# Optimization experiments

Measured on AMD Instinct MI355X. Metric: run time of the kernel, lower is better.

The kernel has to match this reference:

```python
import jax, jax.numpy as jnp
import numpy as np

B, S, H, DIN, DOUT = 4, 2048, 8, 128, 128


def setup_inputs() -> dict:
    key = jax.random.key(0)
    ks = jax.random.split(key, 11)
    sc = 0.05
    return {
        "q": jax.random.normal(ks[0], (B, S, DIN), jnp.float32),
        "k": jax.random.normal(ks[1], (B, S, DIN), jnp.float32),
        "v": jax.random.normal(ks[2], (B, S, DOUT), jnp.float32),
        "Wq": jax.random.normal(ks[3], (DIN, DIN * H), jnp.float32) * sc,
        "bq": jax.random.normal(ks[4], (DIN * H,), jnp.float32) * sc,
        "Wk": jax.random.normal(ks[5], (DIN, DIN * H), jnp.float32) * sc,
        "bk": jax.random.normal(ks[6], (DIN * H,), jnp.float32) * sc,
        "Wv": jax.random.normal(ks[7], (DOUT, DOUT * H), jnp.float32) * sc,
        "bv": jax.random.normal(ks[8], (DOUT * H,), jnp.float32) * sc,
        "Wo": jax.random.normal(ks[9], (H * DOUT, DOUT), jnp.float32) * sc,
        "bo": jax.random.normal(ks[10], (DOUT,), jnp.float32) * sc,
    }


def reference(q, k, v, Wq, bq, Wk, bk, Wv, bv, Wo, bo):
    b, s, din = q.shape
    dout = v.shape[-1]
    h = Wq.shape[1] // din
    # project and split heads: [B, S, H, D] -> [B, H, S, D]
    qs = (q @ Wq + bq).reshape(b, s, h, din).transpose(0, 2, 1, 3)
    kh = (k @ Wk + bk).reshape(b, k.shape[1], h, din).transpose(0, 2, 1, 3)
    vh = (v @ Wv + bv).reshape(b, v.shape[1], h, dout).transpose(0, 2, 1, 3)
    # scaled dot-product attention; note the original scales by sqrt(input_dim)
    scale = 1.0 / jnp.sqrt(jnp.asarray(din, q.dtype))
    scores = jnp.einsum("bhqd,bhkd->bhqk", qs, kh) * scale
    attn = jax.nn.softmax(scores, axis=-1)
    out = jnp.einsum("bhqk,bhkd->bhqd", attn, vh)  # [B, H, S, Dout]
    out = out.transpose(0, 2, 1, 3).reshape(b, s, h * dout)
    return out @ Wo + bo
```

## Files before the change

kernel.cpp:

```cpp
#include <hip/hip_runtime.h>
#include <hip/hip_bf16.h>
#include <stdint.h>

typedef __bf16 bf16_t;
typedef bf16_t bf16x8 __attribute__((ext_vector_type(8)));
typedef bf16_t bf16x4 __attribute__((ext_vector_type(4)));
typedef float  f32x4  __attribute__((ext_vector_type(4)));

#define MFMA_BF16 __builtin_amdgcn_mfma_f32_16x16x32_bf16

constexpr int BB = 4, SS = 2048, HH = 8;
constexpr float QK_SCALE = 0.08838834764831845f;
constexpr float LOG2E    = 1.4426950408889634f;
constexpr float QSCL     = QK_SCALE * LOG2E;

__device__ __forceinline__ float exp2_fast(float x) {
#if __has_builtin(__builtin_amdgcn_exp2f)
    return __builtin_amdgcn_exp2f(x);
#else
    return __expf(x * 0.6931471805599453f);
#endif
}

__device__ __forceinline__ void dma16(const bf16_t* g, bf16_t* l) {
    __builtin_amdgcn_global_load_lds(
        (const __attribute__((address_space(1))) void*)g,
        (__attribute__((address_space(3))) void*)l, 16, 0, 0);
}

__global__ void prep_kernel(const float* __restrict__ q, const float* __restrict__ k,
                            const float* __restrict__ v,
                            const float* __restrict__ Wq, const float* __restrict__ Wk,
                            const float* __restrict__ Wv, const float* __restrict__ Wo,
                            bf16_t* __restrict__ WqT, bf16_t* __restrict__ WkT,
                            bf16_t* __restrict__ WvT, bf16_t* __restrict__ WoT,
                            bf16_t* __restrict__ Abf)
{
    int bid = blockIdx.x, t = threadIdx.x;
    if (bid < 128) {
        __shared__ float tile[64][65];
        int m = bid >> 5, tl = bid & 31;
        const float* src; bf16_t* dst; int R, C, tr, tc; float scale = 1.0f;
        if (m < 3) {
            src = (m == 0) ? Wq : (m == 1) ? Wk : Wv;
            dst = (m == 0) ? WqT : (m == 1) ? WkT : WvT;
            R = 128; C = 1024; tr = tl >> 4; tc = tl & 15;
            if (m == 0) scale = QSCL;
        } else {
            src = Wo; dst = WoT; R = 1024; C = 128; tr = tl >> 1; tc = tl & 1;
        }
        int r0 = tr * 64, c0 = tc * 64;
        int rr = t >> 2, cc = (t & 3) * 16;
        const float4* s4 = (const float4*)(src + (size_t)(r0 + rr) * C + c0 + cc);
        #pragma unroll
        for (int i = 0; i < 4; ++i) {
            float4 f = s4[i];
            tile[rr][cc + 4 * i + 0] = f.x; tile[rr][cc + 4 * i + 1] = f.y;
            tile[rr][cc + 4 * i + 2] = f.z; tile[rr][cc + 4 * i + 3] = f.w;
        }
        __syncthreads();
        bf16x8 o0, o1;
        #pragma unroll
        for (int i = 0; i < 8; ++i) o0[i] = (bf16_t)(tile[cc + i][rr] * scale);
        #pragma unroll
        for (int i = 0; i < 8; ++i) o1[i] = (bf16_t)(tile[cc + 8 + i][rr] * scale);
        bf16_t* d = dst + (size_t)(c0 + rr) * R + r0 + cc;
        *(bf16x8*)d = o0;
        *(bf16x8*)(d + 8) = o1;
    } else {
        int bid2 = bid - 128;
        size_t base = (size_t)bid2 * 4096 + t * 16;
        int z = (int)(base >> 20);
        size_t off = base & 1048575;
        const float* s = (z == 0) ? q : (z == 1) ? k : v;
        const float4* s4 = (const float4*)(s + off);
        bf16_t* d = Abf + (size_t)z * 1048576 + off;
        float4 f0 = s4[0], f1 = s4[1], f2 = s4[2], f3 = s4[3];
        bf16x8 p0 = { (bf16_t)f0.x, (bf16_t)f0.y, (bf16_t)f0.z, (bf16_t)f0.w,
                      (bf16_t)f1.x, (bf16_t)f1.y, (bf16_t)f1.z, (bf16_t)f1.w };
        bf16x8 p1 = { (bf16_t)f2.x, (bf16_t)f2.y, (bf16_t)f2.z, (bf16_t)f2.w,
                      (bf16_t)f3.x, (bf16_t)f3.y, (bf16_t)f3.z, (bf16_t)f3.w };
        *(bf16x8*)d = p0;
        *(bf16x8*)(d + 8) = p1;
    }
}

__global__ __launch_bounds__(256, 2)
void proj_kernel(const bf16_t* __restrict__ Abf,
                 const bf16_t* __restrict__ WqT, const bf16_t* __restrict__ WkT,
                 const bf16_t* __restrict__ WvT,
                 const float* __restrict__ bq, const float* __restrict__ bk,
                 const float* __restrict__ bv,
                 bf16_t* __restrict__ Qh, bf16_t* __restrict__ Kh, bf16_t* __restrict__ VhT)
{
    __shared__ __align__(16) bf16_t a_s[2][128 * 64];
    __shared__ __align__(16) bf16_t b_s[2][128 * 64];
    const int z = blockIdx.z;
    const bf16_t* A    = Abf + (size_t)z * 1048576;
    const bf16_t* BT   = (z == 0) ? WqT : (z == 1) ? WkT : WvT;
    const float*  bias = (z == 0) ? bq  : (z == 1) ? bk  : bv;
    const float   bscale = (z == 0) ? QSCL : 1.0f;
    const int t = threadIdx.x, w = t >> 6, lane = t & 63, q = lane >> 4, ln = lane & 15;
    const int m0 = blockIdx.x * 128;
    const int n0 = blockIdx.y * 128;
    const int wm = (w & 1) * 64, wn = (w >> 1) * 64;

    auto stage = [&](int buf, int kb) {
        #pragma unroll
        for (int j = 0; j < 4; ++j) {
            int row = w * 32 + j * 8 + (lane >> 3);
            int u = (lane & 7) ^ (row & 7);
            dma16(A + (size_t)(m0 + row) * 128 + kb * 64 + u * 8,
                  &a_s[buf][(w * 32 + j * 8) * 64]);
            dma16(BT + (size_t)(n0 + row) * 128 + kb * 64 + u * 8,
                  &b_s[buf][(w * 32 + j * 8) * 64]);
        }
    };

    f32x4 acc[4][4] = {};
    stage(0, 0);
    __syncthreads();
    stage(1, 1);
    #pragma unroll
    for (int kb = 0; kb < 2; ++kb) {
        if (kb == 1) __syncthreads();
        const bf16_t* as = a_s[kb];
        const bf16_t* bs = b_s[kb];
        #pragma unroll
        for (int kc = 0; kc < 2; ++kc) {
            bf16x8 af[4], bfr[4];
            #pragma unroll
            for (int mi = 0; mi < 4; ++mi)
                af[mi] = *(const bf16x8*)&as[(wm + mi * 16 + ln) * 64 + (((kc * 4 + q) ^ (ln & 7)) * 8)];
            #pragma unroll
            for (int ni = 0; ni < 4; ++ni)
                bfr[ni] = *(const bf16x8*)&bs[(wn + ni * 16 + ln) * 64 + (((kc * 4 + q) ^ (ln & 7)) * 8)];
            if (z != 2) {
                #pragma unroll
                for (int mi = 0; mi < 4; ++mi)
                    #pragma unroll
                    for (int ni = 0; ni < 4; ++ni)
                        acc[mi][ni] = MFMA_BF16(af[mi], bfr[ni], acc[mi][ni], 0, 0, 0);
            } else {
                #pragma unroll
                for (int mi = 0; mi < 4; ++mi)
                    #pragma unroll
                    for (int ni = 0; ni < 4; ++ni)
                        acc[mi][ni] = MFMA_BF16(bfr[ni], af[mi], acc[mi][ni], 0, 0, 0);
            }
        }
    }
    bf16_t* out = (z == 0) ? Qh : (z == 1) ? Kh : VhT;
    if (z != 2) {
        #pragma unroll
        for (int ni = 0; ni < 4; ++ni) {
            int col = n0 + wn + ni * 16 + ln;
            int h = col >> 7, d = col & 127;
            float bvv = bias[col] * bscale;
            #pragma unroll
            for (int mi = 0; mi < 4; ++mi) {
                int mbase = m0 + wm + mi * 16 + q * 4;
                int b = mbase >> 11, s = mbase & 2047;
                #pragma unroll
                for (int r = 0; r < 4; ++r)
                    out[((size_t)(b * HH + h) * SS + (s + r)) * 128 + d] =
                        (bf16_t)(acc[mi][ni][r] + bvv);
            }
        }
    } else {
        #pragma unroll
        for (int ni = 0; ni < 4; ++ni) {
            #pragma unroll
            for (int r = 0; r < 4; ++r) {
                int col = n0 + wn + ni * 16 + q * 4 + r;
                int h = col >> 7, d = col & 127;
                float bvv = bias[col];
                #pragma unroll
                for (int mi = 0; mi < 4; ++mi) {
                    int mg = m0 + wm + mi * 16 + ln;
                    int b = mg >> 11, s = mg & 2047;
                    out[((size_t)(b * HH + h) * 128 + d) * SS + s] =
                        (bf16_t)(acc[mi][ni][r] + bvv);
                }
            }
        }
    }
}

__global__ __launch_bounds__(256, 2)
void attn_kernel(const bf16_t* __restrict__ Qh, const bf16_t* __restrict__ Kh,
                 const bf16_t* __restrict__ VhT, bf16_t* __restrict__ Aout)
{
    __shared__ __align__(16) bf16_t k_s[2][64 * 128];
    __shared__ __align__(16) bf16_t v_s[2][128 * 64];
    __shared__ __align__(16) bf16_t p_s[4 * 32 * 64];
    const int t = threadIdx.x;
    const int w = t >> 6, lane = t & 63, q = lane >> 4, ln = lane & 15;
    const int bh = blockIdx.y;
    const int q0 = blockIdx.x * 128;
    const size_t hb = (size_t)bh * SS * 128;

    bf16x8 qf[2][4];
    #pragma unroll
    for (int rg = 0; rg < 2; ++rg) {
        const bf16_t* qrow = Qh + hb + (size_t)(q0 + w * 32 + rg * 16 + ln) * 128;
        #pragma unroll
        for (int kc = 0; kc < 4; ++kc)
            qf[rg][kc] = *(const bf16x8*)(qrow + kc * 32 + q * 8);
    }
    const bf16_t one = (bf16_t)1.0f;
    bf16x8 ones = { one, one, one, one, one, one, one, one };
    f32x4 o[2][8] = {};
    f32x4 ol[2] = {};
    bf16_t* pw = &p_s[w * 32 * 64];

    auto stage = [&](int buf, int kv0) {
        #pragma unroll
        for (int j = 0; j < 4; ++j) {
            int row = w * 16 + j * 4 + (lane >> 4);
            int blk = (lane & 15) ^ (row & 7);
            dma16(Kh + hb + (size_t)(kv0 + row) * 128 + blk * 8,
                  &k_s[buf][(w * 16 + j * 4) * 128]);
        }
        #pragma unroll
        for (int j = 0; j < 4; ++j) {
            int row = w * 32 + j * 8 + (lane >> 3);
            int blk = (lane & 7) ^ (row & 7);
            dma16(VhT + hb + (size_t)row * SS + kv0 + blk * 8,
                  &v_s[buf][(w * 32 + j * 8) * 64]);
        }
    };

    stage(0, 0);
    for (int it = 0; it < SS / 64; ++it) {
        int cur = it & 1;
        __syncthreads();
        if (it + 1 < SS / 64) stage(cur ^ 1, (it + 1) * 64);
        const bf16_t* ks = &k_s[cur][0];
        const bf16_t* vs = &v_s[cur][0];
        f32x4 sc[2][4] = {};
        #pragma unroll
        for (int kc = 0; kc < 4; ++kc) {
            #pragma unroll
            for (int nt = 0; nt < 4; ++nt) {
                int row = nt * 16 + ln;
                bf16x8 kf = *(const bf16x8*)&ks[row * 128 + (((kc * 4 + q) ^ (ln & 7)) * 8)];
                sc[0][nt] = MFMA_BF16(kf, qf[0][kc], sc[0][nt], 0, 0, 0);
                sc[1][nt] = MFMA_BF16(kf, qf[1][kc], sc[1][nt], 0, 0, 0);
            }
        }
        #pragma unroll
        for (int rg = 0; rg < 2; ++rg) {
            #pragma unroll
            for (int nt = 0; nt < 4; ++nt) {
                bf16x4 pk;
                #pragma unroll
                for (int r = 0; r < 4; ++r)
                    pk[r] = (bf16_t)exp2_fast(sc[rg][nt][r]);
                int row = rg * 16 + ln;
                int blk = (2 * nt + (q >> 1)) ^ (row & 7);
                *(bf16x4*)&pw[row * 64 + blk * 8 + (q & 1) * 4] = pk;
            }
        }
        #pragma unroll
        for (int c2 = 0; c2 < 2; ++c2) {
            int pblk = (c2 * 4 + q) ^ (ln & 7);
            bf16x8 pf0 = *(const bf16x8*)&pw[ln * 64 + pblk * 8];
            bf16x8 pf1 = *(const bf16x8*)&pw[(16 + ln) * 64 + pblk * 8];
            ol[0] = MFMA_BF16(pf0, ones, ol[0], 0, 0, 0);
            ol[1] = MFMA_BF16(pf1, ones, ol[1], 0, 0, 0);
            #pragma unroll
            for (int dt = 0; dt < 8; ++dt) {
                int vrow = dt * 16 + ln;
                bf16x8 vf = *(const bf16x8*)&vs[vrow * 64 + (((c2 * 4 + q) ^ (ln & 7)) * 8)];
                o[0][dt] = MFMA_BF16(pf0, vf, o[0][dt], 0, 0, 0);
                o[1][dt] = MFMA_BF16(pf1, vf, o[1][dt], 0, 0, 0);
            }
        }
    }
    const int b = bh >> 3, h = bh & 7;
    #pragma unroll
    for (int rg = 0; rg < 2; ++rg) {
        #pragma unroll
        for (int r = 0; r < 4; ++r) {
            float inv = 1.0f / ol[rg][r];
            int s = q0 + w * 32 + rg * 16 + q * 4 + r;
            bf16_t* dst = Aout + ((size_t)(b * SS + s)) * 1024 + h * 128;
            #pragma unroll
            for (int dt = 0; dt < 8; ++dt)
                dst[dt * 16 + ln] = (bf16_t)(o[rg][dt][r] * inv);
        }
    }
}

__global__ __launch_bounds__(256, 2)
void out_gemm(const bf16_t* __restrict__ A, const bf16_t* __restrict__ BT,
              const float* __restrict__ bias, float* __restrict__ out)
{
    __shared__ __align__(16) bf16_t a_s[2][32 * 64];
    __shared__ __align__(16) bf16_t b_s[2][128 * 64];
    const int t = threadIdx.x, w = t >> 6, lane = t & 63, q = lane >> 4, ln = lane & 15;
    const int m0 = blockIdx.x * 32;
    const int mh = (w & 1) * 16, nh = (w >> 1) * 64;
    f32x4 acc[4] = {};

    auto stage = [&](int buf, int kk) {
        {
            int row = w * 8 + (lane >> 3);
            int u = (lane & 7) ^ (row & 7);
            dma16(A + (size_t)(m0 + row) * 1024 + kk + u * 8, &a_s[buf][(w * 8) * 64]);
        }
        #pragma unroll
        for (int j = 0; j < 4; ++j) {
            int row = w * 32 + j * 8 + (lane >> 3);
            int u = (lane & 7) ^ (row & 7);
            dma16(BT + (size_t)row * 1024 + kk + u * 8, &b_s[buf][(w * 32 + j * 8) * 64]);
        }
    };

    stage(0, 0);
    for (int kb = 0; kb < 16; ++kb) {
        __syncthreads();
        if (kb < 15) stage((kb + 1) & 1, (kb + 1) * 64);
        const bf16_t* as = a_s[kb & 1];
        const bf16_t* bs = b_s[kb & 1];
        #pragma unroll
        for (int kc = 0; kc < 2; ++kc) {
            bf16x8 af = *(const bf16x8*)&as[(mh + ln) * 64 + (((kc * 4 + q) ^ (ln & 7)) * 8)];
            #pragma unroll
            for (int ni = 0; ni < 4; ++ni) {
                int brow = nh + ni * 16 + ln;
                bf16x8 bfr = *(const bf16x8*)&bs[brow * 64 + (((kc * 4 + q) ^ (ln & 7)) * 8)];
                acc[ni] = MFMA_BF16(af, bfr, acc[ni], 0, 0, 0);
            }
        }
    }
    #pragma unroll
    for (int ni = 0; ni < 4; ++ni) {
        int col = nh + ni * 16 + ln;
        float bv = bias[col];
        #pragma unroll
        for (int r = 0; r < 4; ++r)
            out[(size_t)(m0 + mh + q * 4 + r) * 128 + col] = acc[ni][r] + bv;
    }
}

extern "C" void kernel_launch(void* const* d_in, const int* in_sizes, int n_in,
                              void* d_out, int out_size, void* d_ws, size_t ws_size,
                              hipStream_t stream)
{
    const float* q  = (const float*)d_in[0];
    const float* k  = (const float*)d_in[1];
    const float* v  = (const float*)d_in[2];
    const float* Wq = (const float*)d_in[3];
    const float* bq = (const float*)d_in[4];
    const float* Wk = (const float*)d_in[5];
    const float* bk = (const float*)d_in[6];
    const float* Wv = (const float*)d_in[7];
    const float* bv = (const float*)d_in[8];
    const float* Wo = (const float*)d_in[9];
    const float* bo = (const float*)d_in[10];
    float* out = (float*)d_out;

    char* ws = (char*)d_ws;
    bf16_t* WqT  = (bf16_t*)(ws + 0 * (1 << 18));
    bf16_t* WkT  = (bf16_t*)(ws + 1 * (1 << 18));
    bf16_t* WvT  = (bf16_t*)(ws + 2 * (1 << 18));
    bf16_t* WoT  = (bf16_t*)(ws + 3 * (1 << 18));
    bf16_t* Abf  = (bf16_t*)(ws + (1 << 20));
    bf16_t* Qh   = (bf16_t*)(ws + (1 << 23));
    bf16_t* Kh   = (bf16_t*)(ws + (1 << 23) + 1 * (1 << 24));
    bf16_t* VhT  = (bf16_t*)(ws + (1 << 23) + 2 * (1 << 24));
    bf16_t* Aout = (bf16_t*)(ws + (1 << 23) + 3 * (1 << 24));

    prep_kernel<<<896, 256, 0, stream>>>(q, k, v, Wq, Wk, Wv, Wo,
                                         WqT, WkT, WvT, WoT, Abf);
    proj_kernel<<<dim3(64, 8, 3), 256, 0, stream>>>(Abf, WqT, WkT, WvT,
                                                    bq, bk, bv, Qh, Kh, VhT);
    attn_kernel<<<dim3(SS / 128, BB * HH), 256, 0, stream>>>(Qh, Kh, VhT, Aout);
    out_gemm<<<256, 256, 0, stream>>>(Aout, WoT, bo, out);
}
```

Before: 185.6 us.

## Use 32x32 MFMA in attention with 256-query tiles and LDS-staged projection stores

The attention kernel moves from 16x16x32 to 32x32x16 bf16 MFMA, with each wave handling 64 query rows and each block 256. The row sum is accumulated in registers from the exponentials, replacing the extra ones-MFMA. The projection kernel now stages its output tile through LDS so global stores are coalesced 16-byte vectors, including the transposed V layout. The aim is to raise MFMA efficiency and cut scattered store traffic, at the cost of a larger register footprint, occupancy lowered to one block, and fewer blocks in the grid.

```diff
diff --git a/kernel.cpp b/kernel.cpp
--- a/kernel.cpp
+++ b/kernel.cpp
@@ -6,8 +6,10 @@
 typedef bf16_t bf16x8 __attribute__((ext_vector_type(8)));
 typedef bf16_t bf16x4 __attribute__((ext_vector_type(4)));
 typedef float  f32x4  __attribute__((ext_vector_type(4)));
+typedef float  f32x16 __attribute__((ext_vector_type(16)));
 
 #define MFMA_BF16 __builtin_amdgcn_mfma_f32_16x16x32_bf16
+#define MFMA32    __builtin_amdgcn_mfma_f32_32x32x16_bf16
 
 constexpr int BB = 4, SS = 2048, HH = 8;
 constexpr float QK_SCALE = 0.08838834764831845f;
@@ -93,8 +95,7 @@
                  const float* __restrict__ bv,
                  bf16_t* __restrict__ Qh, bf16_t* __restrict__ Kh, bf16_t* __restrict__ VhT)
 {
-    __shared__ __align__(16) bf16_t a_s[2][128 * 64];
-    __shared__ __align__(16) bf16_t b_s[2][128 * 64];
+    __shared__ __align__(16) bf16_t smem[2 * 2 * 128 * 64];
     const int z = blockIdx.z;
     const bf16_t* A    = Abf + (size_t)z * 1048576;
     const bf16_t* BT   = (z == 0) ? WqT : (z == 1) ? WkT : WvT;
@@ -106,14 +107,16 @@
     const int wm = (w & 1) * 64, wn = (w >> 1) * 64;
 
     auto stage = [&](int buf, int kb) {
+        bf16_t* as = smem + buf * 16384;
+        bf16_t* bs = smem + buf * 16384 + 8192;
         #pragma unroll
         for (int j = 0; j < 4; ++j) {
             int row = w * 32 + j * 8 + (lane >> 3);
             int u = (lane & 7) ^ (row & 7);
             dma16(A + (size_t)(m0 + row) * 128 + kb * 64 + u * 8,
-                  &a_s[buf][(w * 32 + j * 8) * 64]);
+                  &as[(w * 32 + j * 8) * 64]);
             dma16(BT + (size_t)(n0 + row) * 128 + kb * 64 + u * 8,
-                  &b_s[buf][(w * 32 + j * 8) * 64]);
+                  &bs[(w * 32 + j * 8) * 64]);
         }
     };
 
@@ -124,8 +127,8 @@
     #pragma unroll
     for (int kb = 0; kb < 2; ++kb) {
         if (kb == 1) __syncthreads();
-        const bf16_t* as = a_s[kb];
-        const bf16_t* bs = b_s[kb];
+        const bf16_t* as = smem + kb * 16384;
+        const bf16_t* bs = smem + kb * 16384 + 8192;
         #pragma unroll
         for (int kc = 0; kc < 2; ++kc) {
             bf16x8 af[4], bfr[4];
@@ -135,160 +138,170 @@
             #pragma unroll
             for (int ni = 0; ni < 4; ++ni)
                 bfr[ni] = *(const bf16x8*)&bs[(wn + ni * 16 + ln) * 64 + (((kc * 4 + q) ^ (ln & 7)) * 8)];
-            if (z != 2) {
+            #pragma unroll
+            for (int mi = 0; mi < 4; ++mi)
                 #pragma unroll
-                for (int mi = 0; mi < 4; ++mi)
-                    #pragma unroll
-                    for (int ni = 0; ni < 4; ++ni)
-                        acc[mi][ni] = MFMA_BF16(af[mi], bfr[ni], acc[mi][ni], 0, 0, 0);
-            } else {
-                #pragma unroll
-                for (int mi = 0; mi < 4; ++mi)
-                    #pragma unroll
-                    for (int ni = 0; ni < 4; ++ni)
-                        acc[mi][ni] = MFMA_BF16(bfr[ni], af[mi], acc[mi][ni], 0, 0, 0);
-            }
-        }
-    }
-    bf16_t* out = (z == 0) ? Qh : (z == 1) ? Kh : VhT;
-    if (z != 2) {
-        #pragma unroll
-        for (int ni = 0; ni < 4; ++ni) {
-            int col = n0 + wn + ni * 16 + ln;
-            int h = col >> 7, d = col & 127;
-            float bvv = bias[col] * bscale;
-            #pragma unroll
-            for (int mi = 0; mi < 4; ++mi) {
-                int mbase = m0 + wm + mi * 16 + q * 4;
-                int b = mbase >> 11, s = mbase & 2047;
-                #pragma unroll
-                for (int r = 0; r < 4; ++r)
-                    out[((size_t)(b * HH + h) * SS + (s + r)) * 128 + d] =
-                        (bf16_t)(acc[mi][ni][r] + bvv);
-            }
-        }
-    } else {
-        #pragma unroll
-        for (int ni = 0; ni < 4; ++ni) {
+                for (int ni = 0; ni < 4; ++ni)
+                    acc[mi][ni] = MFMA_BF16(af[mi], bfr[ni], acc[mi][ni], 0, 0, 0);
+        }
+    }
+    __syncthreads();
+    bf16_t* tb = smem;
+    #pragma unroll
+    for (int ni = 0; ni < 4; ++ni) {
+        int col = wn + ni * 16 + ln;
+        float bvv = bias[n0 + col] * bscale;
+        #pragma unroll
+        for (int mi = 0; mi < 4; ++mi) {
             #pragma unroll
             for (int r = 0; r < 4; ++r) {
-                int col = n0 + wn + ni * 16 + q * 4 + r;
-                int h = col >> 7, d = col & 127;
-                float bvv = bias[col];
-                #pragma unroll
-                for (int mi = 0; mi < 4; ++mi) {
-                    int mg = m0 + wm + mi * 16 + ln;
-                    int b = mg >> 11, s = mg & 2047;
-                    out[((size_t)(b * HH + h) * 128 + d) * SS + s] =
-                        (bf16_t)(acc[mi][ni][r] + bvv);
-                }
-            }
-        }
-    }
-}
-
-__global__ __launch_bounds__(256, 2)
+                int rowm = wm + mi * 16 + q * 4 + r;
+                bf16_t val = (bf16_t)(acc[mi][ni][r] + bvv);
+                if (z != 2) tb[rowm * 136 + col] = val;
+                else        tb[col * 136 + rowm] = val;
+            }
+        }
+    }
+    __syncthreads();
+    {
+        int row = t >> 1, half = t & 1;
+        const bf16_t* src = tb + row * 136 + half * 64;
+        const int b = m0 >> 11, s0 = m0 & 2047, h = n0 >> 7;
+        bf16_t* dst;
+        if (z != 2)
+            dst = ((z == 0) ? Qh : Kh) + ((size_t)((b * HH + h) * SS) + s0 + row) * 128 + half * 64;
+        else
+            dst = VhT + ((size_t)((b * HH + h) * 128 + row)) * SS + s0 + half * 64;
+        #pragma unroll
+        for (int i = 0; i < 8; ++i)
+            *(bf16x8*)(dst + i * 8) = *(const bf16x8*)(src + i * 8);
+    }
+}
+
+__global__ __launch_bounds__(256, 1)
 void attn_kernel(const bf16_t* __restrict__ Qh, const bf16_t* __restrict__ Kh,
                  const bf16_t* __restrict__ VhT, bf16_t* __restrict__ Aout)
 {
     __shared__ __align__(16) bf16_t k_s[2][64 * 128];
     __shared__ __align__(16) bf16_t v_s[2][128 * 64];
-    __shared__ __align__(16) bf16_t p_s[4 * 32 * 64];
+    __shared__ __align__(16) bf16_t p_s[4][64 * 64];
+    __shared__ float l_lds[4][64];
     const int t = threadIdx.x;
-    const int w = t >> 6, lane = t & 63, q = lane >> 4, ln = lane & 15;
+    const int w = t >> 6, lane = t & 63;
+    const int hh = lane >> 5, l31 = lane & 31;
     const int bh = blockIdx.y;
-    const int q0 = blockIdx.x * 128;
+    const int q0 = blockIdx.x * 256;
+    const int qw0 = q0 + w * 64;
     const size_t hb = (size_t)bh * SS * 128;
 
-    bf16x8 qf[2][4];
-    #pragma unroll
-    for (int rg = 0; rg < 2; ++rg) {
-        const bf16_t* qrow = Qh + hb + (size_t)(q0 + w * 32 + rg * 16 + ln) * 128;
-        #pragma unroll
-        for (int kc = 0; kc < 4; ++kc)
-            qf[rg][kc] = *(const bf16x8*)(qrow + kc * 32 + q * 8);
-    }
-    const bf16_t one = (bf16_t)1.0f;
-    bf16x8 ones = { one, one, one, one, one, one, one, one };
-    f32x4 o[2][8] = {};
-    f32x4 ol[2] = {};
-    bf16_t* pw = &p_s[w * 32 * 64];
+    bf16x8 qf[2][8];
+    #pragma unroll
+    for (int ni = 0; ni < 2; ++ni) {
+        const bf16_t* qrow = Qh + hb + (size_t)(qw0 + ni * 32 + l31) * 128 + hh * 8;
+        #pragma unroll
+        for (int c = 0; c < 8; ++c)
+            qf[ni][c] = *(const bf16x8*)(qrow + c * 16);
+    }
+    f32x16 o[2][4] = {};
+    float lsum[2] = {0.f, 0.f};
+    bf16_t* pw = p_s[w];
 
     auto stage = [&](int buf, int kv0) {
         #pragma unroll
         for (int j = 0; j < 4; ++j) {
             int row = w * 16 + j * 4 + (lane >> 4);
-            int blk = (lane & 15) ^ (row & 7);
-            dma16(Kh + hb + (size_t)(kv0 + row) * 128 + blk * 8,
+            int u = (lane & 15) ^ (row & 15);
+            dma16(Kh + hb + (size_t)(kv0 + row) * 128 + u * 8,
                   &k_s[buf][(w * 16 + j * 4) * 128]);
         }
         #pragma unroll
         for (int j = 0; j < 4; ++j) {
             int row = w * 32 + j * 8 + (lane >> 3);
-            int blk = (lane & 7) ^ (row & 7);
-            dma16(VhT + hb + (size_t)row * SS + kv0 + blk * 8,
+            int u = (lane & 7) ^ (row & 7);
+            dma16(VhT + hb + (size_t)row * SS + kv0 + u * 8,
                   &v_s[buf][(w * 32 + j * 8) * 64]);
         }
     };
 
     stage(0, 0);
     for (int it = 0; it < SS / 64; ++it) {
-        int cur = it & 1;
+        const int cur = it & 1;
         __syncthreads();
         if (it + 1 < SS / 64) stage(cur ^ 1, (it + 1) * 64);
-        const bf16_t* ks = &k_s[cur][0];
-        const bf16_t* vs = &v_s[cur][0];
-        f32x4 sc[2][4] = {};
-        #pragma unroll
-        for (int kc = 0; kc < 4; ++kc) {
-            #pragma unroll
-            for (int nt = 0; nt < 4; ++nt) {
-                int row = nt * 16 + ln;
-                bf16x8 kf = *(const bf16x8*)&ks[row * 128 + (((kc * 4 + q) ^ (ln & 7)) * 8)];
-                sc[0][nt] = MFMA_BF16(kf, qf[0][kc], sc[0][nt], 0, 0, 0);
-                sc[1][nt] = MFMA_BF16(kf, qf[1][kc], sc[1][nt], 0, 0, 0);
-            }
-        }
-        #pragma unroll
-        for (int rg = 0; rg < 2; ++rg) {
-            #pragma unroll
-            for (int nt = 0; nt < 4; ++nt) {
-                bf16x4 pk;
+        const bf16_t* ks = k_s[cur];
+        const bf16_t* vs = v_s[cur];
+
+        #pragma unroll
+        for (int mi = 0; mi < 2; ++mi) {
+            const int krow = mi * 32 + l31;
+            const bf16_t* kb = ks + krow * 128;
+            const int ksw = krow & 15;
+            f32x16 s0 = {}, s1 = {};
+            #pragma unroll
+            for (int c = 0; c < 8; ++c) {
+                bf16x8 kf = *(const bf16x8*)&kb[((2 * c + hh) ^ ksw) * 8];
+                s0 = MFMA32(kf, qf[0][c], s0, 0, 0, 0);
+                s1 = MFMA32(kf, qf[1][c], s1, 0, 0, 0);
+            }
+            const int psw = l31 & 7;
+            #pragma unroll
+            for (int ni = 0; ni < 2; ++ni) {
+                const f32x16 sv = ni ? s1 : s0;
+                bf16_t* prow = pw + (ni * 32 + l31) * 64 + hh * 4;
+                float ls = 0.f;
                 #pragma unroll
-                for (int r = 0; r < 4; ++r)
-                    pk[r] = (bf16_t)exp2_fast(sc[rg][nt][r]);
-                int row = rg * 16 + ln;
-                int blk = (2 * nt + (q >> 1)) ^ (row & 7);
-                *(bf16x4*)&pw[row * 64 + blk * 8 + (q & 1) * 4] = pk;
-            }
-        }
-        #pragma unroll
-        for (int c2 = 0; c2 < 2; ++c2) {
-            int pblk = (c2 * 4 + q) ^ (ln & 7);
-            bf16x8 pf0 = *(const bf16x8*)&pw[ln * 64 + pblk * 8];
-            bf16x8 pf1 = *(const bf16x8*)&pw[(16 + ln) * 64 + pblk * 8];
-            ol[0] = MFMA_BF16(pf0, ones, ol[0], 0, 0, 0);
-            ol[1] = MFMA_BF16(pf1, ones, ol[1], 0, 0, 0);
-            #pragma unroll
-            for (int dt = 0; dt < 8; ++dt) {
-                int vrow = dt * 16 + ln;
-                bf16x8 vf = *(const bf16x8*)&vs[vrow * 64 + (((c2 * 4 + q) ^ (ln & 7)) * 8)];
-                o[0][dt] = MFMA_BF16(pf0, vf, o[0][dt], 0, 0, 0);
-                o[1][dt] = MFMA_BF16(pf1, vf, o[1][dt], 0, 0, 0);
-            }
-        }
-    }
-    const int b = bh >> 3, h = bh & 7;
-    #pragma unroll
-    for (int rg = 0; rg < 2; ++rg) {
-        #pragma unroll
-        for (int r = 0; r < 4; ++r) {
-            float inv = 1.0f / ol[rg][r];
-            int s = q0 + w * 32 + rg * 16 + q * 4 + r;
-            bf16_t* dst = Aout + ((size_t)(b * SS + s)) * 1024 + h * 128;
-            #pragma unroll
-            for (int dt = 0; dt < 8; ++dt)
-                dst[dt * 16 + ln] = (bf16_t)(o[rg][dt][r] * inv);
+                for (int g = 0; g < 4; ++g) {
+                    bf16x4 pk;
+                    #pragma unroll
+                    for (int r = 0; r < 4; ++r) {
+                        float e = exp2_fast(sv[g * 4 + r]);
+                        ls += e;
+                        pk[r] = (bf16_t)e;
+                    }
+                    *(bf16x4*)&prow[((mi * 4 + g) ^ psw) * 8] = pk;
+                }
+                lsum[ni] += ls;
+            }
+        }
+        #pragma unroll
+        for (int c = 0; c < 4; ++c) {
+            bf16x8 vf[4];
+            #pragma unroll
+            for (int ni = 0; ni < 4; ++ni) {
+                int drow = ni * 32 + l31;
+                vf[ni] = *(const bf16x8*)&vs[drow * 64 + (((2 * c + hh) ^ (drow & 7)) * 8)];
+            }
+            #pragma unroll
+            for (int mp = 0; mp < 2; ++mp) {
+                int prow = mp * 32 + l31;
+                bf16x8 pf = *(const bf16x8*)&pw[prow * 64 + (((2 * c + hh) ^ (prow & 7)) * 8)];
+                #pragma unroll
+                for (int ni = 0; ni < 4; ++ni)
+                    o[mp][ni] = MFMA32(pf, vf[ni], o[mp][ni], 0, 0, 0);
+            }
+        }
+    }
+    lsum[0] += __shfl_xor(lsum[0], 32);
+    lsum[1] += __shfl_xor(lsum[1], 32);
+    if (hh == 0) {
+        l_lds[w][l31] = lsum[0];
+        l_lds[w][32 + l31] = lsum[1];
+    }
+    const int b = bh >> 3, hd = bh & 7;
+    #pragma unroll
+    for (int mp = 0; mp < 2; ++mp) {
+        #pragma unroll
+        for (int g = 0; g < 4; ++g) {
+            #pragma unroll
+            for (int r = 0; r < 4; ++r) {
+                int qrl = mp * 32 + g * 8 + hh * 4 + r;
+                float inv = 1.0f / l_lds[w][qrl];
+                int s = qw0 + qrl;
+                bf16_t* dst = Aout + ((size_t)(b * SS + s)) * 1024 + hd * 128;
+                #pragma unroll
+                for (int ni = 0; ni < 4; ++ni)
+                    dst[ni * 32 + l31] = (bf16_t)(o[mp][ni][g * 4 + r] * inv);
+            }
         }
     }
 }
@@ -377,6 +390,6 @@
                                          WqT, WkT, WvT, WoT, Abf);
     proj_kernel<<<dim3(64, 8, 3), 256, 0, stream>>>(Abf, WqT, WkT, WvT,
                                                     bq, bk, bv, Qh, Kh, VhT);
-    attn_kernel<<<dim3(SS / 128, BB * HH), 256, 0, stream>>>(Qh, Kh, VhT, Aout);
+    attn_kernel<<<dim3(SS / 256, BB * HH), 256, 0, stream>>>(Qh, Kh, VhT, Aout);
     out_gemm<<<256, 256, 0, stream>>>(Aout, WoT, bo, out);
 }
```

New measurement: 223.0 us. 20.2% more time.

## Split attention KV tile across warp pairs with smem reduction; shrink out_gemm tiles

Applied to the files above, without the earlier changes.

The attention kernel now pairs warps so each pair shares 64 query rows and splits each 64-key tile into two 32-key halves. This lets each K fragment load feed four query row groups instead of two, and the partial outputs and row sums are combined through shared memory at the end. Register pressure rises (o becomes 4x8 f32x4 per warp) and an extra reduction pass is added. Separately, out_gemm uses 16-row tiles with 512 blocks and a higher occupancy hint, aiming for more parallelism on the small output GEMM.

```diff
diff --git a/kernel.cpp b/kernel.cpp
--- a/kernel.cpp
+++ b/kernel.cpp
@@ -191,124 +191,158 @@
 void attn_kernel(const bf16_t* __restrict__ Qh, const bf16_t* __restrict__ Kh,
                  const bf16_t* __restrict__ VhT, bf16_t* __restrict__ Aout)
 {
-    __shared__ __align__(16) bf16_t k_s[2][64 * 128];
-    __shared__ __align__(16) bf16_t v_s[2][128 * 64];
-    __shared__ __align__(16) bf16_t p_s[4 * 32 * 64];
+    __shared__ __align__(16) bf16_t smem[40960];
+    bf16_t* k_s = smem;
+    bf16_t* v_s = smem + 16384;
+    bf16_t* pw  = smem + 32768 + (threadIdx.x >> 6) * 2048;
     const int t = threadIdx.x;
     const int w = t >> 6, lane = t & 63, q = lane >> 4, ln = lane & 15;
+    const int qh = w >> 1, kh = w & 1;
     const int bh = blockIdx.y;
     const int q0 = blockIdx.x * 128;
     const size_t hb = (size_t)bh * SS * 128;
 
-    bf16x8 qf[2][4];
+    bf16x8 qf[4][4];
     #pragma unroll
-    for (int rg = 0; rg < 2; ++rg) {
-        const bf16_t* qrow = Qh + hb + (size_t)(q0 + w * 32 + rg * 16 + ln) * 128;
+    for (int rg = 0; rg < 4; ++rg) {
+        const bf16_t* qp = Qh + hb + (size_t)(q0 + qh * 64 + rg * 16 + ln) * 128;
         #pragma unroll
         for (int kc = 0; kc < 4; ++kc)
-            qf[rg][kc] = *(const bf16x8*)(qrow + kc * 32 + q * 8);
+            qf[rg][kc] = *(const bf16x8*)(qp + kc * 32 + q * 8);
     }
     const bf16_t one = (bf16_t)1.0f;
     bf16x8 ones = { one, one, one, one, one, one, one, one };
-    f32x4 o[2][8] = {};
-    f32x4 ol[2] = {};
-    bf16_t* pw = &p_s[w * 32 * 64];
+    f32x4 o[4][8] = {};
+    f32x4 ol[4] = {};
 
     auto stage = [&](int buf, int kv0) {
         #pragma unroll
         for (int j = 0; j < 4; ++j) {
             int row = w * 16 + j * 4 + (lane >> 4);
-            int blk = (lane & 15) ^ (row & 7);
-            dma16(Kh + hb + (size_t)(kv0 + row) * 128 + blk * 8,
-                  &k_s[buf][(w * 16 + j * 4) * 128]);
+            int u = (lane & 15) ^ (row & 7);
+            dma16(Kh + hb + (size_t)(kv0 + row) * 128 + u * 8,
+                  &k_s[buf * 8192 + (w * 16 + j * 4) * 128]);
         }
         #pragma unroll
         for (int j = 0; j < 4; ++j) {
             int row = w * 32 + j * 8 + (lane >> 3);
-            int blk = (lane & 7) ^ (row & 7);
-            dma16(VhT + hb + (size_t)row * SS + kv0 + blk * 8,
-                  &v_s[buf][(w * 32 + j * 8) * 64]);
+            int u = (lane & 7) ^ (row & 7);
+            dma16(VhT + hb + (size_t)row * SS + kv0 + u * 8,
+                  &v_s[buf * 8192 + (w * 32 + j * 8) * 64]);
         }
     };
 
     stage(0, 0);
     for (int it = 0; it < SS / 64; ++it) {
-        int cur = it & 1;
+        const int cur = it & 1;
         __syncthreads();
         if (it + 1 < SS / 64) stage(cur ^ 1, (it + 1) * 64);
-        const bf16_t* ks = &k_s[cur][0];
-        const bf16_t* vs = &v_s[cur][0];
-        f32x4 sc[2][4] = {};
-        #pragma unroll
-        for (int kc = 0; kc < 4; ++kc) {
-            #pragma unroll
-            for (int nt = 0; nt < 4; ++nt) {
-                int row = nt * 16 + ln;
-                bf16x8 kf = *(const bf16x8*)&ks[row * 128 + (((kc * 4 + q) ^ (ln & 7)) * 8)];
-                sc[0][nt] = MFMA_BF16(kf, qf[0][kc], sc[0][nt], 0, 0, 0);
-                sc[1][nt] = MFMA_BF16(kf, qf[1][kc], sc[1][nt], 0, 0, 0);
-            }
-        }
-        #pragma unroll
-        for (int rg = 0; rg < 2; ++rg) {
-            #pragma unroll
-            for (int nt = 0; nt < 4; ++nt) {
+        const bf16_t* ks = &k_s[cur * 8192];
+        const bf16_t* vs = &v_s[cur * 8192];
+
+        #pragma unroll
+        for (int nt = 0; nt < 2; ++nt) {
+            const int krow = kh * 32 + nt * 16 + ln;
+            const bf16_t* kp = ks + krow * 128;
+            const int ksw = krow & 7;
+            f32x4 sc[4] = {};
+            #pragma unroll
+            for (int kc = 0; kc < 4; ++kc) {
+                bf16x8 kf = *(const bf16x8*)(kp + ((kc * 4 + q) ^ ksw) * 8);
+                #pragma unroll
+                for (int rg = 0; rg < 4; ++rg)
+                    sc[rg] = MFMA_BF16(kf, qf[rg][kc], sc[rg], 0, 0, 0);
+            }
+            #pragma unroll
+            for (int rg = 0; rg < 4; ++rg) {
                 bf16x4 pk;
                 #pragma unroll
                 for (int r = 0; r < 4; ++r)
-                    pk[r] = (bf16_t)exp2_fast(sc[rg][nt][r]);
-                int row = rg * 16 + ln;
-                int blk = (2 * nt + (q >> 1)) ^ (row & 7);
-                *(bf16x4*)&pw[row * 64 + blk * 8 + (q & 1) * 4] = pk;
-            }
-        }
-        #pragma unroll
-        for (int c2 = 0; c2 < 2; ++c2) {
-            int pblk = (c2 * 4 + q) ^ (ln & 7);
-            bf16x8 pf0 = *(const bf16x8*)&pw[ln * 64 + pblk * 8];
-            bf16x8 pf1 = *(const bf16x8*)&pw[(16 + ln) * 64 + pblk * 8];
-            ol[0] = MFMA_BF16(pf0, ones, ol[0], 0, 0, 0);
-            ol[1] = MFMA_BF16(pf1, ones, ol[1], 0, 0, 0);
+                    pk[r] = (bf16_t)exp2_fast(sc[rg][r]);
+                int prow = rg * 16 + ln;
+                int u = (nt * 2 + (q >> 1)) ^ (prow & 3);
+                *(bf16x4*)&pw[prow * 32 + u * 8 + (q & 1) * 4] = pk;
+            }
+        }
+        bf16x8 pf[4];
+        #pragma unroll
+        for (int mp = 0; mp < 4; ++mp) {
+            int prow = mp * 16 + ln;
+            pf[mp] = *(const bf16x8*)&pw[prow * 32 + (q ^ (prow & 3)) * 8];
+            ol[mp] = MFMA_BF16(pf[mp], ones, ol[mp], 0, 0, 0);
+        }
+        #pragma unroll
+        for (int dt = 0; dt < 8; ++dt) {
+            int vrow = dt * 16 + ln;
+            bf16x8 vf = *(const bf16x8*)&vs[vrow * 64 + (((kh * 4 + q) ^ (vrow & 7)) * 8)];
+            #pragma unroll
+            for (int mp = 0; mp < 4; ++mp)
+                o[mp][dt] = MFMA_BF16(pf[mp], vf, o[mp][dt], 0, 0, 0);
+        }
+    }
+    __syncthreads();
+    float* ored = (float*)smem;
+    float* lred = (float*)(smem + 32768);
+    if (ln == 0) {
+        #pragma unroll
+        for (int mp = 0; mp < 4; ++mp)
+            *(f32x4*)&lred[w * 64 + mp * 16 + q * 4] = ol[mp];
+    }
+    if (kh == 1) {
+        float* dst = ored + qh * 8192;
+        #pragma unroll
+        for (int mp = 0; mp < 4; ++mp)
             #pragma unroll
             for (int dt = 0; dt < 8; ++dt) {
-                int vrow = dt * 16 + ln;
-                bf16x8 vf = *(const bf16x8*)&vs[vrow * 64 + (((c2 * 4 + q) ^ (ln & 7)) * 8)];
-                o[0][dt] = MFMA_BF16(pf0, vf, o[0][dt], 0, 0, 0);
-                o[1][dt] = MFMA_BF16(pf1, vf, o[1][dt], 0, 0, 0);
-            }
-        }
-    }
-    const int b = bh >> 3, h = bh & 7;
-    #pragma unroll
-    for (int rg = 0; rg < 2; ++rg) {
-        #pragma unroll
-        for (int r = 0; r < 4; ++r) {
-            float inv = 1.0f / ol[rg][r];
-            int s = q0 + w * 32 + rg * 16 + q * 4 + r;
-            bf16_t* dst = Aout + ((size_t)(b * SS + s)) * 1024 + h * 128;
-            #pragma unroll
-            for (int dt = 0; dt < 8; ++dt)
-                dst[dt * 16 + ln] = (bf16_t)(o[rg][dt][r] * inv);
-        }
-    }
-}
-
-__global__ __launch_bounds__(256, 2)
+                int drow = dt * 16 + ln;
+                int u = (mp * 4 + q) ^ ln;
+                *(f32x4*)&dst[drow * 64 + u * 4] = o[mp][dt];
+            }
+    }
+    __syncthreads();
+    if (kh == 0) {
+        const int b = bh >> 3, hd = bh & 7;
+        const float* src = ored + qh * 8192;
+        #pragma unroll
+        for (int mp = 0; mp < 4; ++mp) {
+            f32x4 lp = *(const f32x4*)&lred[(w + 1) * 64 + mp * 16 + q * 4];
+            f32x4 inv;
+            #pragma unroll
+            for (int r = 0; r < 4; ++r) inv[r] = 1.0f / (ol[mp][r] + lp[r]);
+            #pragma unroll
+            for (int dt = 0; dt < 8; ++dt) {
+                int drow = dt * 16 + ln;
+                int u = (mp * 4 + q) ^ ln;
+                f32x4 op = *(const f32x4*)&src[drow * 64 + u * 4];
+                int sbase = q0 + qh * 64 + mp * 16 + q * 4;
+                #pragma unroll
+                for (int r = 0; r < 4; ++r)
+                    Aout[((size_t)(b * SS + sbase + r)) * 1024 + hd * 128 + drow] =
+                        (bf16_t)((o[mp][dt][r] + op[r]) * inv[r]);
+            }
+        }
+    }
+}
+
+__global__ __launch_bounds__(256, 4)
 void out_gemm(const bf16_t* __restrict__ A, const bf16_t* __restrict__ BT,
               const float* __restrict__ bias, float* __restrict__ out)
 {
-    __shared__ __align__(16) bf16_t a_s[2][32 * 64];
+    __shared__ __align__(16) bf16_t a_s[2][16 * 64];
     __shared__ __align__(16) bf16_t b_s[2][128 * 64];
     const int t = threadIdx.x, w = t >> 6, lane = t & 63, q = lane >> 4, ln = lane & 15;
-    const int m0 = blockIdx.x * 32;
-    const int mh = (w & 1) * 16, nh = (w >> 1) * 64;
-    f32x4 acc[4] = {};
+    const int m0 = blockIdx.x * 16;
+    const int nh = w * 32;
+    f32x4 acc[2] = {};
 
     auto stage = [&](int buf, int kk) {
-        {
-            int row = w * 8 + (lane >> 3);
-            int u = (lane & 7) ^ (row & 7);
-            dma16(A + (size_t)(m0 + row) * 1024 + kk + u * 8, &a_s[buf][(w * 8) * 64]);
+        if (w == 0) {
+            #pragma unroll
+            for (int j = 0; j < 2; ++j) {
+                int row = j * 8 + (lane >> 3);
+                int u = (lane & 7) ^ (row & 7);
+                dma16(A + (size_t)(m0 + row) * 1024 + kk + u * 8, &a_s[buf][(j * 8) * 64]);
+            }
         }
         #pragma unroll
         for (int j = 0; j < 4; ++j) {
@@ -326,9 +360,9 @@
         const bf16_t* bs = b_s[kb & 1];
         #pragma unroll
         for (int kc = 0; kc < 2; ++kc) {
-            bf16x8 af = *(const bf16x8*)&as[(mh + ln) * 64 + (((kc * 4 + q) ^ (ln & 7)) * 8)];
-            #pragma unroll
-            for (int ni = 0; ni < 4; ++ni) {
+            bf16x8 af = *(const bf16x8*)&as[ln * 64 + (((kc * 4 + q) ^ (ln & 7)) * 8)];
+            #pragma unroll
+            for (int ni = 0; ni < 2; ++ni) {
                 int brow = nh + ni * 16 + ln;
                 bf16x8 bfr = *(const bf16x8*)&bs[brow * 64 + (((kc * 4 + q) ^ (ln & 7)) * 8)];
                 acc[ni] = MFMA_BF16(af, bfr, acc[ni], 0, 0, 0);
@@ -336,12 +370,12 @@
         }
     }
     #pragma unroll
-    for (int ni = 0; ni < 4; ++ni) {
+    for (int ni = 0; ni < 2; ++ni) {
         int col = nh + ni * 16 + ln;
         float bv = bias[col];
         #pragma unroll
         for (int r = 0; r < 4; ++r)
-            out[(size_t)(m0 + mh + q * 4 + r) * 128 + col] = acc[ni][r] + bv;
+            out[(size_t)(m0 + q * 4 + r) * 128 + col] = acc[ni][r] + bv;
     }
 }
 
@@ -378,5 +412,5 @@
     proj_kernel<<<dim3(64, 8, 3), 256, 0, stream>>>(Abf, WqT, WkT, WvT,
                                                     bq, bk, bv, Qh, Kh, VhT);
     attn_kernel<<<dim3(SS / 128, BB * HH), 256, 0, stream>>>(Qh, Kh, VhT, Aout);
-    out_gemm<<<256, 256, 0, stream>>>(Aout, WoT, bo, out);
-}
+    out_gemm<<<512, 256, 0, stream>>>(Aout, WoT, bo, out);
+}
```

Measured after the change: 220.4 us. 1.19x slower.
